# Optimization experiments

Hardware: AMD Instinct MI355X
Metric: run time of the kernel (lower is better)

The kernel has to match this reference:

```python
import jax, jax.numpy as jnp
import numpy as np

B, F, D = 4096, 512, 512


def setup_inputs() -> dict:
    key = jax.random.key(0)
    k1, k2, k3 = jax.random.split(key, 3)
    inputs = jax.random.normal(k1, (B, D), dtype=jnp.float32)
    mu = jax.random.normal(k2, (F, D), dtype=jnp.float32)        # exp_mu, random_normal init
    sigma = jax.random.normal(k3, (1, F, D), dtype=jnp.float32)  # exp_sigma, random_normal init
    temperature = jnp.array(2.0, dtype=jnp.float32)              # learned scalar, init 2.0
    return {"inputs": inputs, "mu": mu, "sigma": sigma, "temperature": temperature}


def reference(inputs, mu, sigma, temperature):
    # diff: [B, F, D] broadcast difference (the large fusable intermediate)
    diff = inputs[:, None, :] - mu[None, :, :]
    # scaled L2 norm over feature dim -> [B, F]
    dist = jnp.sqrt(jnp.sum(jnp.square(diff * sigma), axis=-1))
    loc = jnp.exp(-dist)
    # adaptive-temperature softmax gating over formulas
    return jax.nn.softmax(jax.nn.sigmoid(temperature) * loc, axis=-1)
```

## Files before the change

kernel.cpp:

```cpp
#include <hip/hip_runtime.h>
#include <hip/hip_bf16.h>
#include <stdint.h>

#define BB 4096
#define FF 512
#define DD 512
#define KDIM 1024

typedef __bf16 bf16x8 __attribute__((ext_vector_type(8)));
typedef float f32x4 __attribute__((ext_vector_type(4)));
typedef unsigned short u16x8 __attribute__((ext_vector_type(8)));

__device__ __forceinline__ unsigned short f2bf(float f) {
  unsigned u = __builtin_bit_cast(unsigned, f);
  u += 0x7FFFu + ((u >> 16) & 1u);
  return (unsigned short)(u >> 16);
}

__device__ __forceinline__ void async16(const void* g, void* l) {
  auto gp = reinterpret_cast<const __attribute__((address_space(1))) uint32_t*>(
      reinterpret_cast<uintptr_t>(g));
  auto lp = reinterpret_cast<__attribute__((address_space(3))) uint32_t*>(
      reinterpret_cast<uintptr_t>(l));
  __builtin_amdgcn_global_load_lds(gp, lp, 16, 0, 0);
}

__global__ __launch_bounds__(256) void prep_kernel(
    const float* __restrict__ x, const float* __restrict__ mu,
    const float* __restrict__ sg, unsigned short* __restrict__ A,
    unsigned short* __restrict__ W, float* __restrict__ c) {
  __shared__ float red[4];
  const int bid = blockIdx.x;
  const int t = threadIdx.x;
  if (bid < FF) {
    const int f = bid;
    float part = 0.f;
#pragma unroll
    for (int dd = 0; dd < 2; ++dd) {
      const int d = t + dd * 256;
      const float m = mu[f * DD + d];
      const float s = sg[f * DD + d];
      const float s2 = s * s;
      W[f * KDIM + d] = f2bf(s2);
      W[f * KDIM + DD + d] = f2bf(-2.f * s2 * m);
      part += s2 * m * m;
    }
#pragma unroll
    for (int off = 32; off > 0; off >>= 1) part += __shfl_down(part, off, 64);
    const int lane = t & 63, wave = t >> 6;
    if (lane == 0) red[wave] = part;
    __syncthreads();
    if (t == 0) c[f] = red[0] + red[1] + red[2] + red[3];
  } else {
    const int gid = (bid - FF) * 256 + t;
    const int i8 = gid * 8;
    const float4 v0 = *(const float4*)(x + i8);
    const float4 v1 = *(const float4*)(x + i8 + 4);
    const int b = i8 >> 9;
    const int d = i8 & 511;
    u16x8 q2, q1;
    q2[0] = f2bf(v0.x * v0.x); q2[1] = f2bf(v0.y * v0.y);
    q2[2] = f2bf(v0.z * v0.z); q2[3] = f2bf(v0.w * v0.w);
    q2[4] = f2bf(v1.x * v1.x); q2[5] = f2bf(v1.y * v1.y);
    q2[6] = f2bf(v1.z * v1.z); q2[7] = f2bf(v1.w * v1.w);
    q1[0] = f2bf(v0.x); q1[1] = f2bf(v0.y); q1[2] = f2bf(v0.z); q1[3] = f2bf(v0.w);
    q1[4] = f2bf(v1.x); q1[5] = f2bf(v1.y); q1[6] = f2bf(v1.z); q1[7] = f2bf(v1.w);
    *(u16x8*)(A + (size_t)b * KDIM + d) = q2;
    *(u16x8*)(A + (size_t)b * KDIM + DD + d) = q1;
  }
}

__global__ __launch_bounds__(256) void gemm_kernel(
    const unsigned short* __restrict__ A, const unsigned short* __restrict__ W,
    const float* __restrict__ c, float* __restrict__ out) {
  __shared__ __align__(16) unsigned short As[2][64 * 64];
  const int bid = blockIdx.x;
  const int xcd = bid & 7;
  const int k8 = bid >> 3;
  const int m0 = (xcd * 8 + (k8 & 7)) * 64;
  const int n0 = (k8 >> 3) * 128;
  const int tid = threadIdx.x;
  const int lane = tid & 63;
  const int wave = tid >> 6;

  f32x4 acc[4][2];
#pragma unroll
  for (int i = 0; i < 4; ++i)
#pragma unroll
    for (int j = 0; j < 2; ++j) acc[i][j] = (f32x4){0.f, 0.f, 0.f, 0.f};

  const int srow = lane >> 3;
  const int sc16 = lane & 7;
  const int gcol = (sc16 ^ srow) * 8;
  const int quad = lane >> 4;
  const int r = lane & 15;
  const int wn = wave * 32;

  const unsigned short* ag = A + (size_t)(m0 + wave * 16 + srow) * KDIM + gcol;
  const int arb = wave * 16;
  const unsigned short* wg0 = W + (size_t)(n0 + wn + r) * KDIM + quad * 8;

#pragma unroll
  for (int tI = 0; tI < 2; ++tI)
    async16(ag + (size_t)tI * 8 * KDIM, &As[0][(arb + tI * 8) * 64]);

  bf16x8 bc[2][2], bn[2][2];
  bc[0][0] = *(const bf16x8*)(wg0);
  bc[1][0] = *(const bf16x8*)(wg0 + 32);
  bc[0][1] = *(const bf16x8*)(wg0 + 16 * KDIM);
  bc[1][1] = *(const bf16x8*)(wg0 + 16 * KDIM + 32);

#pragma unroll
  for (int kt = 0; kt < KDIM / 64; ++kt) {
    const int cur = kt & 1;
    __syncthreads();
    if (kt + 1 < KDIM / 64) {
      const int k1 = (kt + 1) * 64;
#pragma unroll
      for (int tI = 0; tI < 2; ++tI)
        async16(ag + (size_t)tI * 8 * KDIM + k1, &As[cur ^ 1][(arb + tI * 8) * 64]);
      bn[0][0] = *(const bf16x8*)(wg0 + k1);
      bn[1][0] = *(const bf16x8*)(wg0 + k1 + 32);
      bn[0][1] = *(const bf16x8*)(wg0 + 16 * KDIM + k1);
      bn[1][1] = *(const bf16x8*)(wg0 + 16 * KDIM + k1 + 32);
    }
#pragma unroll
    for (int kk = 0; kk < 2; ++kk) {
      const int pc = ((kk * 4 + quad) ^ (r & 7)) * 8;
#pragma unroll
      for (int mt = 0; mt < 4; ++mt) {
        bf16x8 a = *(const bf16x8*)&As[cur][(mt * 16 + r) * 64 + pc];
        acc[mt][0] = __builtin_amdgcn_mfma_f32_16x16x32_bf16(a, bc[kk][0], acc[mt][0], 0, 0, 0);
        acc[mt][1] = __builtin_amdgcn_mfma_f32_16x16x32_bf16(a, bc[kk][1], acc[mt][1], 0, 0, 0);
      }
    }
#pragma unroll
    for (int kk = 0; kk < 2; ++kk)
#pragma unroll
      for (int nt = 0; nt < 2; ++nt) bc[kk][nt] = bn[kk][nt];
  }

  const int col = lane & 15;
#pragma unroll
  for (int nt = 0; nt < 2; ++nt) {
    const int f = n0 + wn + nt * 16 + col;
    const float cf = c[f];
#pragma unroll
    for (int mt = 0; mt < 4; ++mt) {
      const int mbase = m0 + mt * 16 + quad * 4;
#pragma unroll
      for (int rr = 0; rr < 4; ++rr) {
        const float d2 = acc[mt][nt][rr] + cf;
        const float loc = __expf(-sqrtf(fmaxf(d2, 0.f)));
        out[(size_t)(mbase + rr) * FF + f] = loc;
      }
    }
  }
}

__global__ __launch_bounds__(256) void softmax_kernel(
    float* __restrict__ out, const float* __restrict__ temp) {
  const int lane = threadIdx.x & 63;
  const int wave = threadIdx.x >> 6;
  const int row = blockIdx.x * 4 + wave;
  const float s = 1.f / (1.f + __expf(-temp[0]));
  float4* p = (float4*)(out + (size_t)row * FF + lane * 8);
  const float4 v0 = p[0];
  const float4 v1 = p[1];
  float l[8] = {v0.x * s, v0.y * s, v0.z * s, v0.w * s,
                v1.x * s, v1.y * s, v1.z * s, v1.w * s};
  float mx = l[0];
#pragma unroll
  for (int i = 1; i < 8; ++i) mx = fmaxf(mx, l[i]);
#pragma unroll
  for (int off = 32; off > 0; off >>= 1) mx = fmaxf(mx, __shfl_xor(mx, off, 64));
  float e[8], sum = 0.f;
#pragma unroll
  for (int i = 0; i < 8; ++i) { e[i] = __expf(l[i] - mx); sum += e[i]; }
#pragma unroll
  for (int off = 32; off > 0; off >>= 1) sum += __shfl_xor(sum, off, 64);
  const float inv = 1.f / sum;
  float4 w0 = {e[0] * inv, e[1] * inv, e[2] * inv, e[3] * inv};
  float4 w1 = {e[4] * inv, e[5] * inv, e[6] * inv, e[7] * inv};
  p[0] = w0; p[1] = w1;
}

__global__ __launch_bounds__(256) void naive_loc(
    const float* __restrict__ x, const float* __restrict__ mu,
    const float* __restrict__ sg, float* __restrict__ out) {
  __shared__ float xs[DD];
  const int b = blockIdx.x;
  for (int d = threadIdx.x; d < DD; d += 256) xs[d] = x[(size_t)b * DD + d];
  __syncthreads();
  for (int f = threadIdx.x; f < FF; f += 256) {
    float acc = 0.f;
    for (int d = 0; d < DD; ++d) {
      const float s = sg[(size_t)f * DD + d];
      const float df = (xs[d] - mu[(size_t)f * DD + d]) * s;
      acc = fmaf(df, df, acc);
    }
    out[(size_t)b * FF + f] = __expf(-sqrtf(acc));
  }
}

extern "C" void kernel_launch(void* const* d_in, const int* in_sizes, int n_in,
                              void* d_out, int out_size, void* d_ws, size_t ws_size,
                              hipStream_t stream) {
  const float* x = (const float*)d_in[0];
  const float* mu = (const float*)d_in[1];
  const float* sg = (const float*)d_in[2];
  const float* temp = (const float*)d_in[3];
  float* out = (float*)d_out;

  const size_t needA = (size_t)BB * KDIM * 2;
  const size_t needW = (size_t)FF * KDIM * 2;
  const size_t needC = (size_t)FF * 4;
  if (ws_size >= needA + needW + needC) {
    unsigned short* A = (unsigned short*)d_ws;
    unsigned short* W = A + (size_t)BB * KDIM;
    float* c = (float*)(W + (size_t)FF * KDIM);
    prep_kernel<<<FF + (BB * DD / 8) / 256, 256, 0, stream>>>(x, mu, sg, A, W, c);
    gemm_kernel<<<256, 256, 0, stream>>>(A, W, c, out);
  } else {
    naive_loc<<<BB, 256, 0, stream>>>(x, mu, sg, out);
  }
  softmax_kernel<<<BB / 4, 256, 0, stream>>>(out, temp);
}
```

Measured before the change: 92.81 us.

## Fuse prep, GEMM and softmax into one cooperative kernel with grid syncs

```diff
diff --git a/kernel.cpp b/kernel.cpp
--- a/kernel.cpp
+++ b/kernel.cpp
@@ -1,6 +1,9 @@
 #include <hip/hip_runtime.h>
+#include <hip/hip_cooperative_groups.h>
 #include <hip/hip_bf16.h>
 #include <stdint.h>
+
+namespace cg = cooperative_groups;
 
 #define BB 4096
 #define FF 512
@@ -23,6 +26,171 @@
   auto lp = reinterpret_cast<__attribute__((address_space(3))) uint32_t*>(
       reinterpret_cast<uintptr_t>(l));
   __builtin_amdgcn_global_load_lds(gp, lp, 16, 0, 0);
+}
+
+__global__ __launch_bounds__(256) void fused_kernel(
+    const float* __restrict__ x, const float* __restrict__ mu,
+    const float* __restrict__ sg, const float* __restrict__ temp,
+    unsigned short* __restrict__ A, unsigned short* __restrict__ W,
+    float* __restrict__ c, float* __restrict__ out) {
+  __shared__ __align__(16) unsigned short As[2][64 * 64];
+  __shared__ float red[4];
+  const int bid = blockIdx.x;
+  const int tid = threadIdx.x;
+  const int lane = tid & 63;
+  const int wave = tid >> 6;
+
+#pragma unroll
+  for (int i = 0; i < 2; ++i) {
+    const int f = bid * 2 + i;
+    float part = 0.f;
+#pragma unroll
+    for (int dd = 0; dd < 2; ++dd) {
+      const int d = tid + dd * 256;
+      const float m = mu[f * DD + d];
+      const float s = sg[f * DD + d];
+      const float s2 = s * s;
+      W[f * KDIM + d] = f2bf(s2);
+      W[f * KDIM + DD + d] = f2bf(-2.f * s2 * m);
+      part += s2 * m * m;
+    }
+#pragma unroll
+    for (int off = 32; off > 0; off >>= 1) part += __shfl_down(part, off, 64);
+    if (lane == 0) red[wave] = part;
+    __syncthreads();
+    if (tid == 0) c[f] = red[0] + red[1] + red[2] + red[3];
+    __syncthreads();
+  }
+#pragma unroll
+  for (int p = 0; p < 4; ++p) {
+    const int gid = bid * 1024 + p * 256 + tid;
+    const int i8 = gid * 8;
+    const float4 v0 = *(const float4*)(x + i8);
+    const float4 v1 = *(const float4*)(x + i8 + 4);
+    const int b = i8 >> 9;
+    const int d = i8 & 511;
+    u16x8 q2, q1;
+    q2[0] = f2bf(v0.x * v0.x); q2[1] = f2bf(v0.y * v0.y);
+    q2[2] = f2bf(v0.z * v0.z); q2[3] = f2bf(v0.w * v0.w);
+    q2[4] = f2bf(v1.x * v1.x); q2[5] = f2bf(v1.y * v1.y);
+    q2[6] = f2bf(v1.z * v1.z); q2[7] = f2bf(v1.w * v1.w);
+    q1[0] = f2bf(v0.x); q1[1] = f2bf(v0.y); q1[2] = f2bf(v0.z); q1[3] = f2bf(v0.w);
+    q1[4] = f2bf(v1.x); q1[5] = f2bf(v1.y); q1[6] = f2bf(v1.z); q1[7] = f2bf(v1.w);
+    *(u16x8*)(A + (size_t)b * KDIM + d) = q2;
+    *(u16x8*)(A + (size_t)b * KDIM + DD + d) = q1;
+  }
+
+  cg::this_grid().sync();
+
+  {
+    const int xcd = bid & 7;
+    const int k8 = bid >> 3;
+    const int m0 = (xcd * 8 + (k8 & 7)) * 64;
+    const int n0 = (k8 >> 3) * 128;
+
+    f32x4 acc[4][2];
+#pragma unroll
+    for (int i = 0; i < 4; ++i)
+#pragma unroll
+      for (int j = 0; j < 2; ++j) acc[i][j] = (f32x4){0.f, 0.f, 0.f, 0.f};
+
+    const int srow = lane >> 3;
+    const int sc16 = lane & 7;
+    const int gcol = (sc16 ^ srow) * 8;
+    const int quad = lane >> 4;
+    const int r = lane & 15;
+    const int wn = wave * 32;
+
+    const unsigned short* ag = A + (size_t)(m0 + wave * 16 + srow) * KDIM + gcol;
+    const int arb = wave * 16;
+    const unsigned short* wg0 = W + (size_t)(n0 + wn + r) * KDIM + quad * 8;
+
+#pragma unroll
+    for (int tI = 0; tI < 2; ++tI)
+      async16(ag + (size_t)tI * 8 * KDIM, &As[0][(arb + tI * 8) * 64]);
+
+    bf16x8 bc[2][2], bn[2][2];
+    bc[0][0] = *(const bf16x8*)(wg0);
+    bc[1][0] = *(const bf16x8*)(wg0 + 32);
+    bc[0][1] = *(const bf16x8*)(wg0 + 16 * KDIM);
+    bc[1][1] = *(const bf16x8*)(wg0 + 16 * KDIM + 32);
+
+#pragma unroll
+    for (int kt = 0; kt < KDIM / 64; ++kt) {
+      const int cur = kt & 1;
+      __syncthreads();
+      if (kt + 1 < KDIM / 64) {
+        const int k1 = (kt + 1) * 64;
+#pragma unroll
+        for (int tI = 0; tI < 2; ++tI)
+          async16(ag + (size_t)tI * 8 * KDIM + k1, &As[cur ^ 1][(arb + tI * 8) * 64]);
+        bn[0][0] = *(const bf16x8*)(wg0 + k1);
+        bn[1][0] = *(const bf16x8*)(wg0 + k1 + 32);
+        bn[0][1] = *(const bf16x8*)(wg0 + 16 * KDIM + k1);
+        bn[1][1] = *(const bf16x8*)(wg0 + 16 * KDIM + k1 + 32);
+      }
+#pragma unroll
+      for (int kk = 0; kk < 2; ++kk) {
+        const int pc = ((kk * 4 + quad) ^ (r & 7)) * 8;
+#pragma unroll
+        for (int mt = 0; mt < 4; ++mt) {
+          bf16x8 a = *(const bf16x8*)&As[cur][(mt * 16 + r) * 64 + pc];
+          acc[mt][0] = __builtin_amdgcn_mfma_f32_16x16x32_bf16(a, bc[kk][0], acc[mt][0], 0, 0, 0);
+          acc[mt][1] = __builtin_amdgcn_mfma_f32_16x16x32_bf16(a, bc[kk][1], acc[mt][1], 0, 0, 0);
+        }
+      }
+#pragma unroll
+      for (int kk = 0; kk < 2; ++kk)
+#pragma unroll
+        for (int nt = 0; nt < 2; ++nt) bc[kk][nt] = bn[kk][nt];
+    }
+
+    const int col = lane & 15;
+#pragma unroll
+    for (int nt = 0; nt < 2; ++nt) {
+      const int f = n0 + wn + nt * 16 + col;
+      const float cf = c[f];
+#pragma unroll
+      for (int mt = 0; mt < 4; ++mt) {
+        const int mbase = m0 + mt * 16 + quad * 4;
+#pragma unroll
+        for (int rr = 0; rr < 4; ++rr) {
+          const float d2 = acc[mt][nt][rr] + cf;
+          const float loc = __expf(-sqrtf(fmaxf(d2, 0.f)));
+          out[(size_t)(mbase + rr) * FF + f] = loc;
+        }
+      }
+    }
+  }
+
+  cg::this_grid().sync();
+
+  {
+    const float s = 1.f / (1.f + __expf(-temp[0]));
+#pragma unroll
+    for (int rr4 = 0; rr4 < 4; ++rr4) {
+      const int row = bid * 16 + wave * 4 + rr4;
+      float4* p = (float4*)(out + (size_t)row * FF + lane * 8);
+      const float4 v0 = p[0];
+      const float4 v1 = p[1];
+      float l[8] = {v0.x * s, v0.y * s, v0.z * s, v0.w * s,
+                    v1.x * s, v1.y * s, v1.z * s, v1.w * s};
+      float mx = l[0];
+#pragma unroll
+      for (int i = 1; i < 8; ++i) mx = fmaxf(mx, l[i]);
+#pragma unroll
+      for (int off = 32; off > 0; off >>= 1) mx = fmaxf(mx, __shfl_xor(mx, off, 64));
+      float e[8], sum = 0.f;
+#pragma unroll
+      for (int i = 0; i < 8; ++i) { e[i] = __expf(l[i] - mx); sum += e[i]; }
+#pragma unroll
+      for (int off = 32; off > 0; off >>= 1) sum += __shfl_xor(sum, off, 64);
+      const float inv = 1.f / sum;
+      float4 w0 = {e[0] * inv, e[1] * inv, e[2] * inv, e[3] * inv};
+      float4 w1 = {e[4] * inv, e[5] * inv, e[6] * inv, e[7] * inv};
+      p[0] = w0; p[1] = w1;
+    }
+  }
 }
 
 __global__ __launch_bounds__(256) void prep_kernel(
@@ -219,10 +387,17 @@
     unsigned short* A = (unsigned short*)d_ws;
     unsigned short* W = A + (size_t)BB * KDIM;
     float* c = (float*)(W + (size_t)FF * KDIM);
-    prep_kernel<<<FF + (BB * DD / 8) / 256, 256, 0, stream>>>(x, mu, sg, A, W, c);
-    gemm_kernel<<<256, 256, 0, stream>>>(A, W, c, out);
+    void* args[8] = {(void*)&x, (void*)&mu, (void*)&sg, (void*)&temp,
+                     (void*)&A, (void*)&W, (void*)&c, (void*)&out};
+    hipError_t e = hipLaunchCooperativeKernel(
+        (const void*)fused_kernel, dim3(256), dim3(256), args, 0u, stream);
+    if (e != hipSuccess) {
+      prep_kernel<<<FF + (BB * DD / 8) / 256, 256, 0, stream>>>(x, mu, sg, A, W, c);
+      gemm_kernel<<<256, 256, 0, stream>>>(A, W, c, out);
+      softmax_kernel<<<BB / 4, 256, 0, stream>>>(out, temp);
+    }
   } else {
     naive_loc<<<BB, 256, 0, stream>>>(x, mu, sg, out);
-  }
-  softmax_kernel<<<BB / 4, 256, 0, stream>>>(out, temp);
-}
+    softmax_kernel<<<BB / 4, 256, 0, stream>>>(out, temp);
+  }
+}
```

Result: slower. 169.5 us (+82.7%).
